# Performance work log

Hardware: AMD Instinct MI355X
Metric: run time of the kernel (lower is better)

Reference implementation:

```python
import jax, jax.numpy as jnp
import numpy as np
from jax.scipy.special import logsumexp

N = 4096          # nodes per graph
E = 65536         # edges per graph
HID = 128
HEADS = 4
HD = HID // HEADS
L_GNN = 2
L_CROSS = 3
SINK_ITERS = 20
LN_EPS = 1e-5
SCALE = 1.0 / np.sqrt(HD)


def layer_norm(x, g, b):
    m = jnp.mean(x, axis=-1, keepdims=True)
    v = jnp.mean((x - m) ** 2, axis=-1, keepdims=True)
    return (x - m) * jax.lax.rsqrt(v + LN_EPS) * g + b


def gcn_conv(x, ei, w, b):
    # PyG GCNConv: self-loops + symmetric normalization, sum aggregation
    n = x.shape[0]
    xl = x @ w                                  # [n, hid]
    loops = jnp.arange(n, dtype=ei.dtype)
    src = jnp.concatenate([ei[0], loops])
    dst = jnp.concatenate([ei[1], loops])
    deg = jax.ops.segment_sum(jnp.ones_like(src, dtype=x.dtype), dst, num_segments=n)
    dinv = jnp.where(deg > 0, jax.lax.rsqrt(deg), 0.0)
    norm = dinv[src] * dinv[dst]                # [E+n]
    msg = xl[src] * norm[:, None]
    return jax.ops.segment_sum(msg, dst, num_segments=n) + b


def encode(x, ei, gcn_w, gcn_b, ln_g, ln_b):
    h = x
    for l in range(L_GNN):
        h = gcn_conv(h, ei, gcn_w[l], gcn_b[l])
        h = layer_norm(h, ln_g[l], ln_b[l])
        h = jax.nn.relu(h)
    return h


def attend(X, Y, wq, wk, wv, wo, bo):
    # X attends to Y; residual add
    n, m = X.shape[0], Y.shape[0]
    Q = (X @ wq).reshape(n, HEADS, HD).transpose(1, 0, 2)   # [h, n, d]
    K = (Y @ wk).reshape(m, HEADS, HD).transpose(1, 0, 2)
    V = (Y @ wv).reshape(m, HEADS, HD).transpose(1, 0, 2)
    scores = jnp.einsum('hnd,hmd->hnm', Q, K) * SCALE
    attn = jax.nn.softmax(scores, axis=-1)
    O = jnp.einsum('hnm,hmd->hnd', attn, V)                 # [h, n, d]
    O = O.transpose(1, 0, 2).reshape(n, HID)
    return O @ wo + bo + X


def sinkhorn(log_alpha, n_iters=SINK_ITERS):
    def body(i, lp):
        lp = lp - logsumexp(lp, axis=1, keepdims=True)  # row normalize
        lp = lp - logsumexp(lp, axis=0, keepdims=True)  # col normalize
        return lp
    log_p = jax.lax.fori_loop(0, n_iters, body, log_alpha)
    return jnp.exp(log_p)


def setup_inputs() -> dict:
    key = jax.random.key(0)
    ks = jax.random.split(key, 24)
    f32 = jnp.float32
    w = lambda k, *s: jax.random.normal(k, s, dtype=f32) * 0.05
    inp = {
        'A_x': jax.random.normal(ks[0], (N, HID), dtype=f32),
        'A_ei': jax.random.randint(ks[1], (2, E), 0, N),
        'B_x': jax.random.normal(ks[2], (N, HID), dtype=f32),
        'B_ei': jax.random.randint(ks[3], (2, E), 0, N),
        'in_proj_w': w(ks[4], HID, HID),
        'in_proj_b': jnp.zeros((HID,), f32),
        'gcn_w': w(ks[5], L_GNN, HID, HID),
        'gcn_b': jnp.zeros((L_GNN, HID), f32),
        'gcn_ln_g': jnp.ones((L_GNN, HID), f32),
        'gcn_ln_b': jnp.zeros((L_GNN, HID), f32),
        'cross_q': w(ks[6], L_CROSS, HID, HID),
        'cross_k': w(ks[7], L_CROSS, HID, HID),
        'cross_v': w(ks[8], L_CROSS, HID, HID),
        'cross_o': w(ks[9], L_CROSS, HID, HID),
        'cross_o_b': jnp.zeros((L_CROSS, HID), f32),
        'post_ln_g': jnp.ones((HID,), f32),
        'post_ln_b': jnp.zeros((HID,), f32),
        'proj_w': w(ks[10], HID, HID),
        'proj_b': jnp.zeros((HID,), f32),
        'null_vec': jax.random.normal(ks[11], (HID,), dtype=f32) * 0.01,
        'cp_w1': w(ks[12], HID, HID),
        'cp_b1': jnp.zeros((HID,), f32),
        'cp_w2': w(ks[13], HID, HID),
        'cp_b2': jnp.zeros((HID,), f32),
    }
    return inp


def reference(A_x, A_ei, B_x, B_ei, in_proj_w, in_proj_b, gcn_w, gcn_b,
              gcn_ln_g, gcn_ln_b, cross_q, cross_k, cross_v, cross_o,
              cross_o_b, post_ln_g, post_ln_b, proj_w, proj_b, null_vec,
              cp_w1, cp_b1, cp_w2, cp_b2):
    A_in = A_x @ in_proj_w + in_proj_b
    B_in = B_x @ in_proj_w + in_proj_b
    A_h = encode(A_in, A_ei, gcn_w, gcn_b, gcn_ln_g, gcn_ln_b)
    B_h = encode(B_in, B_ei, gcn_w, gcn_b, gcn_ln_g, gcn_ln_b)
    for l in range(L_CROSS):
        A_new = attend(A_h, B_h, cross_q[l], cross_k[l], cross_v[l], cross_o[l], cross_o_b[l])
        B_new = attend(B_h, A_h, cross_q[l], cross_k[l], cross_v[l], cross_o[l], cross_o_b[l])
        A_h, B_h = A_new, B_new
    A_h = layer_norm(A_h, post_ln_g, post_ln_b)
    B_h = layer_norm(B_h, post_ln_g, post_ln_b)
    A_p = A_h @ proj_w + proj_b
    B_p = B_h @ proj_w + proj_b
    inv_sqrt_d = 1.0 / np.sqrt(HID)
    logits = (A_p @ B_p.T) * inv_sqrt_d                    # [N, N]
    null_col = (A_p @ null_vec) * inv_sqrt_d               # [N]
    logits_with_null = jnp.concatenate([logits, null_col[:, None]], axis=1)
    P = sinkhorn(logits_with_null)
    zA = jax.nn.relu(A_p @ cp_w1 + cp_b1) @ cp_w2 + cp_b2
    zB = jax.nn.relu(B_p @ cp_w1 + cp_b1) @ cp_w2 + cp_b2
    return (logits_with_null, P, zA, zB)
```

## Files before the change

### kernel.cpp

```cpp
#include <hip/hip_runtime.h>
#include <hip/hip_bf16.h>
#include <math.h>

#define NN 4096
#define EE 65536
#define HID_ 128
#define HDIM 32
#define NCOL 4097
#define EHP 4104

static constexpr float SCALE_ATT = 0.17677669529663687f;
static constexpr float INV_SQRT_D = 0.08838834764831845f;
static constexpr float LOG2E = 1.4426950408889634f;

typedef __attribute__((ext_vector_type(8))) short bf16x8;
typedef __attribute__((ext_vector_type(4))) float f32x4;
typedef _Float16 half8 __attribute__((ext_vector_type(8)));
typedef _Float16 half2v __attribute__((ext_vector_type(2)));

__device__ __forceinline__ float wred64(float v) {
#pragma unroll
  for (int m = 32; m > 0; m >>= 1) v += __shfl_xor(v, m, 64);
  return v;
}

__device__ __forceinline__ ushort f2b(float f) {
  __hip_bfloat16 h = __float2bfloat16(f);
  union { __hip_bfloat16 h; ushort u; } c;
  c.h = h;
  return c.u;
}

template <bool BIAS, bool RELU, bool RESID>
__global__ __launch_bounds__(256, 2) void gemm128_k(
    const float* __restrict__ x0, const float* __restrict__ x1,
    const float* __restrict__ w, const float* __restrict__ bias,
    const float* __restrict__ res0, const float* __restrict__ res1,
    float* __restrict__ o0, float* __restrict__ o1) {
  const float* x = blockIdx.y ? x1 : x0;
  const float* res = blockIdx.y ? res1 : res0;
  float* out = blockIdx.y ? o1 : o0;
  __shared__ float Xs[32][132];
  __shared__ float Ws[32][128];
  const int tid = threadIdx.x;
  const int rowbase = blockIdx.x * 32;
#pragma unroll
  for (int i = 0; i < 4; ++i) {
    int lin = tid + i * 256;
    int r = lin >> 5, c4 = lin & 31;
    *(float4*)&Xs[r][c4 * 4] =
        *(const float4*)&x[(size_t)(rowbase + r) * HID_ + c4 * 4];
  }
  float acc[4][4] = {};
  const int tr = tid >> 5, tc = tid & 31;
  const int r0 = tr * 4, c0 = tc * 4;
  for (int k0 = 0; k0 < 128; k0 += 32) {
    __syncthreads();
#pragma unroll
    for (int i = 0; i < 4; ++i) {
      int lin = tid + i * 256;
      int r = lin >> 5, c4 = lin & 31;
      *(float4*)&Ws[r][c4 * 4] =
          *(const float4*)&w[(size_t)(k0 + r) * HID_ + c4 * 4];
    }
    __syncthreads();
#pragma unroll
    for (int kk = 0; kk < 32; kk += 4) {
      float4 wv0 = *(const float4*)&Ws[kk + 0][c0];
      float4 wv1 = *(const float4*)&Ws[kk + 1][c0];
      float4 wv2 = *(const float4*)&Ws[kk + 2][c0];
      float4 wv3 = *(const float4*)&Ws[kk + 3][c0];
#pragma unroll
      for (int r = 0; r < 4; ++r) {
        float4 xv = *(const float4*)&Xs[r0 + r][k0 + kk];
        acc[r][0] += xv.x * wv0.x + xv.y * wv1.x + xv.z * wv2.x + xv.w * wv3.x;
        acc[r][1] += xv.x * wv0.y + xv.y * wv1.y + xv.z * wv2.y + xv.w * wv3.y;
        acc[r][2] += xv.x * wv0.z + xv.y * wv1.z + xv.z * wv2.z + xv.w * wv3.z;
        acc[r][3] += xv.x * wv0.w + xv.y * wv1.w + xv.z * wv2.w + xv.w * wv3.w;
      }
    }
  }
  float4 bv = make_float4(0.f, 0.f, 0.f, 0.f);
  if (BIAS) bv = *(const float4*)&bias[c0];
#pragma unroll
  for (int r = 0; r < 4; ++r) {
    size_t orow = (size_t)(rowbase + r0 + r) * HID_ + c0;
    float4 ov;
    ov.x = acc[r][0] + bv.x;
    ov.y = acc[r][1] + bv.y;
    ov.z = acc[r][2] + bv.z;
    ov.w = acc[r][3] + bv.w;
    if (RESID) {
      float4 rv = *(const float4*)&res[orow];
      ov.x += rv.x; ov.y += rv.y; ov.z += rv.z; ov.w += rv.w;
    }
    if (RELU) {
      ov.x = fmaxf(ov.x, 0.f); ov.y = fmaxf(ov.y, 0.f);
      ov.z = fmaxf(ov.z, 0.f); ov.w = fmaxf(ov.w, 0.f);
    }
    *(float4*)&out[orow] = ov;
  }
}

template <int MODE>
__global__ __launch_bounds__(256, 2) void gemm128_bf16_k(
    const float* __restrict__ x0, const float* __restrict__ x1,
    const float* __restrict__ w, float scale, ushort* __restrict__ o0,
    ushort* __restrict__ o1) {
  const float* x = blockIdx.y ? x1 : x0;
  ushort* out = blockIdx.y ? o1 : o0;
  __shared__ float Xs[32][132];
  __shared__ float Ws[32][128];
  const int tid = threadIdx.x;
  const int rowbase = blockIdx.x * 32;
#pragma unroll
  for (int i = 0; i < 4; ++i) {
    int lin = tid + i * 256;
    int r = lin >> 5, c4 = lin & 31;
    *(float4*)&Xs[r][c4 * 4] =
        *(const float4*)&x[(size_t)(rowbase + r) * HID_ + c4 * 4];
  }
  float acc[4][4] = {};
  const int tr = tid >> 5, tc = tid & 31;
  const int r0 = tr * 4, c0 = tc * 4;
  for (int k0 = 0; k0 < 128; k0 += 32) {
    __syncthreads();
#pragma unroll
    for (int i = 0; i < 4; ++i) {
      int lin = tid + i * 256;
      int r = lin >> 5, c4 = lin & 31;
      *(float4*)&Ws[r][c4 * 4] =
          *(const float4*)&w[(size_t)(k0 + r) * HID_ + c4 * 4];
    }
    __syncthreads();
#pragma unroll
    for (int kk = 0; kk < 32; kk += 4) {
      float4 wv0 = *(const float4*)&Ws[kk + 0][c0];
      float4 wv1 = *(const float4*)&Ws[kk + 1][c0];
      float4 wv2 = *(const float4*)&Ws[kk + 2][c0];
      float4 wv3 = *(const float4*)&Ws[kk + 3][c0];
#pragma unroll
      for (int r = 0; r < 4; ++r) {
        float4 xv = *(const float4*)&Xs[r0 + r][k0 + kk];
        acc[r][0] += xv.x * wv0.x + xv.y * wv1.x + xv.z * wv2.x + xv.w * wv3.x;
        acc[r][1] += xv.x * wv0.y + xv.y * wv1.y + xv.z * wv2.y + xv.w * wv3.y;
        acc[r][2] += xv.x * wv0.z + xv.y * wv1.z + xv.z * wv2.z + xv.w * wv3.z;
        acc[r][3] += xv.x * wv0.w + xv.y * wv1.w + xv.z * wv2.w + xv.w * wv3.w;
      }
    }
  }
  if (MODE == 0) {
#pragma unroll
    for (int r = 0; r < 4; ++r) {
      ushort4 pk = make_ushort4(
          f2b(acc[r][0] * scale), f2b(acc[r][1] * scale),
          f2b(acc[r][2] * scale), f2b(acc[r][3] * scale));
      *(ushort4*)&out[(size_t)(rowbase + r0 + r) * HID_ + c0] = pk;
    }
  } else {
#pragma unroll
    for (int r = 0; r < 4; ++r)
#pragma unroll
      for (int c = 0; c < 4; ++c)
        out[(size_t)(c0 + c) * NN + rowbase + r0 + r] = f2b(acc[r][c]);
  }
}

__global__ void count_deg_k(const int* __restrict__ eiA,
                            const int* __restrict__ eiB, int* cntA, int* cntB) {
  int e = blockIdx.x * 256 + threadIdx.x;
  const int* ei = blockIdx.y ? eiB : eiA;
  int* cnt = blockIdx.y ? cntB : cntA;
  atomicAdd(&cnt[ei[EE + e]], 1);
}

__global__ __launch_bounds__(1024) void scan_k(const int* cntA, const int* cntB,
                                               int* rpA, int* rpB, float* dinvA,
                                               float* dinvB) {
  const int* cnt = blockIdx.y ? cntB : cntA;
  int* rp = blockIdx.y ? rpB : rpA;
  float* dinv = blockIdx.y ? dinvB : dinvA;
  __shared__ int part[1024];
  int tid = threadIdx.x;
  int v0 = cnt[tid * 4], v1 = cnt[tid * 4 + 1], v2 = cnt[tid * 4 + 2],
      v3 = cnt[tid * 4 + 3];
  int tot = v0 + v1 + v2 + v3;
  part[tid] = tot;
  __syncthreads();
  int x = tot;
  for (int off = 1; off < 1024; off <<= 1) {
    int y = (tid >= off) ? part[tid - off] : 0;
    __syncthreads();
    x += y;
    part[tid] = x;
    __syncthreads();
  }
  int excl = x - tot;
  rp[tid * 4] = excl;
  rp[tid * 4 + 1] = excl + v0;
  rp[tid * 4 + 2] = excl + v0 + v1;
  rp[tid * 4 + 3] = excl + v0 + v1 + v2;
  if (tid == 1023) rp[4096] = x;
  dinv[tid * 4] = rsqrtf((float)(v0 + 1));
  dinv[tid * 4 + 1] = rsqrtf((float)(v1 + 1));
  dinv[tid * 4 + 2] = rsqrtf((float)(v2 + 1));
  dinv[tid * 4 + 3] = rsqrtf((float)(v3 + 1));
}

__global__ void fill_k(const int* __restrict__ eiA, const int* __restrict__ eiB,
                       const int* rpA, const int* rpB, int* fillA, int* fillB,
                       int* srcA, int* srcB) {
  int e = blockIdx.x * 256 + threadIdx.x;
  const int* ei = blockIdx.y ? eiB : eiA;
  const int* rp = blockIdx.y ? rpB : rpA;
  int* fill = blockIdx.y ? fillB : fillA;
  int* src = blockIdx.y ? srcB : srcA;
  int d = ei[EE + e], s = ei[e];
  int pos = atomicAdd(&fill[d], 1);
  src[rp[d] + pos] = s;
}

__global__ __launch_bounds__(256) void gcn_agg_k(
    const float* __restrict__ xlA, const float* __restrict__ xlB,
    const int* __restrict__ rpA, const int* __restrict__ rpB,
    const int* __restrict__ srcA, const int* __restrict__ srcB,
    const float* __restrict__ dinvA, const float* __restrict__ dinvB,
    const float* __restrict__ gb, const float* __restrict__ lg,
    const float* __restrict__ lb, float* __restrict__ outA,
    float* __restrict__ outB) {
  const float* xl = blockIdx.y ? xlB : xlA;
  const int* rp = blockIdx.y ? rpB : rpA;
  const int* src = blockIdx.y ? srcB : srcA;
  const float* dinv = blockIdx.y ? dinvB : dinvA;
  float* out = blockIdx.y ? outB : outA;
  int wid = threadIdx.x >> 6, lane = threadIdx.x & 63;
  int node = blockIdx.x * 4 + wid;
  int b = rp[node], e = rp[node + 1];
  float di = dinv[node];
  float a0 = 0.f, a1 = 0.f;
  for (int base = b; base < e; base += 64) {
    int rem = e - base;
    int sv = 0;
    float wv = 0.f;
    if (lane < rem) {
      int s = src[base + lane];
      sv = s;
      wv = dinv[s] * di;
    }
    int nch = rem < 64 ? rem : 64;
    for (int j = 0; j < nch; ++j) {
      int s = __shfl(sv, j, 64);
      float w = __shfl(wv, j, 64);
      a0 += xl[(size_t)s * HID_ + lane] * w;
      a1 += xl[(size_t)s * HID_ + 64 + lane] * w;
    }
  }
  a0 += xl[(size_t)node * HID_ + lane] * di * di;
  a1 += xl[(size_t)node * HID_ + 64 + lane] * di * di;
  a0 += gb[lane];
  a1 += gb[64 + lane];
  float mean = wred64(a0 + a1) * (1.f / 128.f);
  float d0 = a0 - mean, d1 = a1 - mean;
  float var = wred64(d0 * d0 + d1 * d1) * (1.f / 128.f);
  float rs = rsqrtf(var + 1e-5f);
  float o0 = d0 * rs * lg[lane] + lb[lane];
  float o1 = d1 * rs * lg[64 + lane] + lb[64 + lane];
  out[(size_t)node * HID_ + lane] = fmaxf(o0, 0.f);
  out[(size_t)node * HID_ + 64 + lane] = fmaxf(o1, 0.f);
}

__global__ __launch_bounds__(256) void ln_k(float* __restrict__ hA,
                                            float* __restrict__ hB,
                                            const float* __restrict__ g,
                                            const float* __restrict__ b) {
  float* h = blockIdx.y ? hB : hA;
  int wid = threadIdx.x >> 6, lane = threadIdx.x & 63;
  int row = blockIdx.x * 4 + wid;
  float a0 = h[(size_t)row * HID_ + lane];
  float a1 = h[(size_t)row * HID_ + 64 + lane];
  float mean = wred64(a0 + a1) * (1.f / 128.f);
  float d0 = a0 - mean, d1 = a1 - mean;
  float var = wred64(d0 * d0 + d1 * d1) * (1.f / 128.f);
  float rs = rsqrtf(var + 1e-5f);
  h[(size_t)row * HID_ + lane] = d0 * rs * g[lane] + b[lane];
  h[(size_t)row * HID_ + 64 + lane] = d1 * rs * g[64 + lane] + b[64 + lane];
}

__global__ __launch_bounds__(256, 2) void attn_mfma_k(
    const ushort* __restrict__ QA, const ushort* __restrict__ KA,
    const ushort* __restrict__ VtA, const ushort* __restrict__ QB,
    const ushort* __restrict__ KB, const ushort* __restrict__ VtB,
    float* __restrict__ outA, float* __restrict__ outB) {
  const int qt = blockIdx.x, h = blockIdx.y, dir = blockIdx.z;
  const ushort* Q = dir ? QB : QA;
  const ushort* K = dir ? KA : KB;
  const ushort* Vt = dir ? VtA : VtB;
  float* out = dir ? outB : outA;

  __shared__ ushort KF[2048];
  __shared__ ushort VF[2048];
  __shared__ ushort PF[4][1024];

  const int tid = threadIdx.x;
  const int w = tid >> 6, l = tid & 63;
  const int lr = l & 15, lg = l >> 4;

  const int qrow = qt * 64 + w * 16 + lr;
  bf16x8 qf = *(const bf16x8*)&Q[(size_t)qrow * HID_ + h * HDIM + lg * 8];

  f32x4 oacc0 = {0.f, 0.f, 0.f, 0.f};
  f32x4 oacc1 = {0.f, 0.f, 0.f, 0.f};
  float lpart = 0.f;

  const int ldst = ((w * 4 + lg) * 16 + lr) * 8;
  const ushort* Kg = K + (size_t)(w * 16 + lr) * HID_ + h * HDIM + lg * 8;
  const ushort* Vg =
      Vt + (size_t)(h * HDIM + (w >> 1) * 16 + lr) * NN + (w & 1) * 32 + lg * 8;

  for (int t = 0; t < 64; ++t) {
    const int kv0 = t * 64;
    __syncthreads();
    *(bf16x8*)&KF[ldst] = *(const bf16x8*)&Kg[(size_t)kv0 * HID_];
    *(bf16x8*)&VF[ldst] = *(const bf16x8*)&Vg[kv0];
    __syncthreads();
#pragma unroll
    for (int s = 0; s < 4; ++s) {
      bf16x8 kf = *(const bf16x8*)&KF[((s * 4 + lg) * 16 + lr) * 8];
      f32x4 c = {0.f, 0.f, 0.f, 0.f};
      c = __builtin_amdgcn_mfma_f32_16x16x32_bf16(kf, qf, c, 0, 0, 0);
      float e0 = exp2f(c[0]), e1 = exp2f(c[1]);
      float e2 = exp2f(c[2]), e3 = exp2f(c[3]);
      lpart += (e0 + e1) + (e2 + e3);
      ushort4 pk = make_ushort4(f2b(e0), f2b(e1), f2b(e2), f2b(e3));
      const int k0 = s >> 1;
      const int lgr = (s & 1) * 2 + (lg >> 1);
      const int e8 = (lg & 1) * 4;
      *(ushort4*)&PF[w][((k0 * 4 + lgr) * 16 + lr) * 8 + e8] = pk;
    }
#pragma unroll
    for (int k0 = 0; k0 < 2; ++k0) {
      bf16x8 pa = *(const bf16x8*)&PF[w][((k0 * 4 + lg) * 16 + lr) * 8];
      bf16x8 vb0 = *(const bf16x8*)&VF[((k0 * 4 + lg) * 16 + lr) * 8];
      bf16x8 vb1 = *(const bf16x8*)&VF[(((2 + k0) * 4 + lg) * 16 + lr) * 8];
      oacc0 = __builtin_amdgcn_mfma_f32_16x16x32_bf16(pa, vb0, oacc0, 0, 0, 0);
      oacc1 = __builtin_amdgcn_mfma_f32_16x16x32_bf16(pa, vb1, oacc1, 0, 0, 0);
    }
  }
  lpart += __shfl_xor(lpart, 16, 64);
  lpart += __shfl_xor(lpart, 32, 64);
#pragma unroll
  for (int r = 0; r < 4; ++r) {
    int q = qt * 64 + w * 16 + lg * 4 + r;
    float ls = __shfl(lpart, lg * 4 + r, 64);
    float inv = 1.f / ls;
    out[(size_t)q * HID_ + h * HDIM + lr] = oacc0[r] * inv;
    out[(size_t)q * HID_ + h * HDIM + 16 + lr] = oacc1[r] * inv;
  }
}

__global__ void castf2b_k(const float* __restrict__ A,
                          const float* __restrict__ B, ushort* __restrict__ Ab,
                          ushort* __restrict__ Bb) {
  int i = (blockIdx.x * 256 + threadIdx.x) * 8;
  float4 a0 = *(const float4*)&A[i];
  float4 a1 = *(const float4*)&A[i + 4];
  *(ushort4*)&Ab[i] = make_ushort4(f2b(a0.x), f2b(a0.y), f2b(a0.z), f2b(a0.w));
  *(ushort4*)&Ab[i + 4] =
      make_ushort4(f2b(a1.x), f2b(a1.y), f2b(a1.z), f2b(a1.w));
  float4 b0 = *(const float4*)&B[i];
  float4 b1 = *(const float4*)&B[i + 4];
  *(ushort4*)&Bb[i] = make_ushort4(f2b(b0.x), f2b(b0.y), f2b(b0.z), f2b(b0.w));
  *(ushort4*)&Bb[i + 4] =
      make_ushort4(f2b(b1.x), f2b(b1.y), f2b(b1.z), f2b(b1.w));
}

__global__ __launch_bounds__(256, 2) void gemm_nt_mfma_k(
    const ushort* __restrict__ Apb, const ushort* __restrict__ Bpb,
    float* __restrict__ L, _Float16* __restrict__ Eh) {
  __shared__ ushort As[128 * 128];
  __shared__ ushort Bs[128 * 128];
  const int tid = threadIdx.x;
  const int ab = blockIdx.y * 128, bb = blockIdx.x * 128;
#pragma unroll
  for (int i = 0; i < 8; ++i) {
    int lin = tid + i * 256;
    int row = lin >> 4, ch = lin & 15;
    int pch = ch ^ (row & 15);
    *(bf16x8*)&As[row * 128 + pch * 8] =
        *(const bf16x8*)&Apb[(size_t)(ab + row) * HID_ + ch * 8];
    *(bf16x8*)&Bs[row * 128 + pch * 8] =
        *(const bf16x8*)&Bpb[(size_t)(bb + row) * HID_ + ch * 8];
  }
  __syncthreads();
  const int w = tid >> 6, l = tid & 63, lr = l & 15, lg = l >> 4;
  f32x4 acc[2][8];
#pragma unroll
  for (int fm = 0; fm < 2; ++fm)
#pragma unroll
    for (int nf = 0; nf < 8; ++nf) acc[fm][nf] = {0.f, 0.f, 0.f, 0.f};
#pragma unroll
  for (int kc = 0; kc < 4; ++kc) {
    bf16x8 a0 = *(const bf16x8*)
        &As[((w * 2 + 0) * 16 + lr) * 128 + ((kc * 4 + lg) ^ lr) * 8];
    bf16x8 a1 = *(const bf16x8*)
        &As[((w * 2 + 1) * 16 + lr) * 128 + ((kc * 4 + lg) ^ lr) * 8];
#pragma unroll
    for (int nf = 0; nf < 8; ++nf) {
      bf16x8 bf = *(const bf16x8*)
          &Bs[(nf * 16 + lr) * 128 + ((kc * 4 + lg) ^ lr) * 8];
      acc[0][nf] = __builtin_amdgcn_mfma_f32_16x16x32_bf16(a0, bf, acc[0][nf], 0, 0, 0);
      acc[1][nf] = __builtin_amdgcn_mfma_f32_16x16x32_bf16(a1, bf, acc[1][nf], 0, 0, 0);
    }
  }
#pragma unroll
  for (int fm = 0; fm < 2; ++fm)
#pragma unroll
    for (int nf = 0; nf < 8; ++nf)
#pragma unroll
      for (int r = 0; r < 4; ++r) {
        int row = ab + (w * 2 + fm) * 16 + lg * 4 + r;
        int col = bb + nf * 16 + lr;
        float v = acc[fm][nf][r] * INV_SQRT_D;
        L[(size_t)row * NCOL + col] = v;
        Eh[(size_t)row * EHP + col] = (_Float16)exp2f(v * LOG2E);
      }
}

__global__ void null_col_k(const float* __restrict__ Ap,
                           const float* __restrict__ nv, float* __restrict__ L,
                           _Float16* __restrict__ Eh) {
  int row = blockIdx.x, lane = threadIdx.x;
  float s = Ap[(size_t)row * HID_ + lane] * nv[lane] +
            Ap[(size_t)row * HID_ + 64 + lane] * nv[64 + lane];
  s = wred64(s);
  if (lane == 0) {
    float v = s * INV_SQRT_D;
    L[(size_t)row * NCOL + 4096] = v;
    Eh[(size_t)row * EHP + 4096] = (_Float16)exp2f(v * LOG2E);
  }
  if (lane >= 1 && lane < 8) Eh[(size_t)row * EHP + 4096 + lane] = (_Float16)0.f;
}

__global__ void sink_init_k(float* t0) {
  int j = blockIdx.x * 256 + threadIdx.x;
  if (j < EHP) t0[j] = 1.f;
}

__global__ __launch_bounds__(256) void sink_rowm_k(
    const _Float16* __restrict__ Eh, const float* __restrict__ t_old,
    float* __restrict__ t_new, float* __restrict__ u) {
  __shared__ float vls[EHP];
  int tid = threadIdx.x;
  if (blockIdx.x < 17) {
    int j = blockIdx.x * 256 + tid;
    if (j < EHP) t_new[j] = 0.f;
  }
  for (int i = tid; i < EHP; i += 256)
    vls[i] = (i < NCOL) ? (1.f / t_old[i]) : 0.f;
  __syncthreads();
  int w = tid >> 6, l = tid & 63;
  for (int rr = 0; rr < 4; ++rr) {
    int row = blockIdx.x * 16 + w * 4 + rr;
    const _Float16* Ep = Eh + (size_t)row * EHP;
    float s = 0.f;
    for (int j = l * 8; j < EHP; j += 512) {
      half8 e = *(const half8*)&Ep[j];
#pragma unroll
      for (int k = 0; k < 8; ++k) s += (float)e[k] * vls[j + k];
    }
    s = wred64(s);
    if (l == 0) u[row] = 1.f / s;
  }
}

__global__ __launch_bounds__(256) void sink_colm_k(
    const _Float16* __restrict__ Eh, const float* __restrict__ u,
    float* __restrict__ t_new) {
  __shared__ float uls[64];
  int tid = threadIdx.x;
  int i0 = blockIdx.y * 64;
  if (tid < 64) uls[tid] = u[i0 + tid];
  __syncthreads();
  int j0 = (blockIdx.x * 256 + tid) * 2;
  if (j0 >= EHP) return;
  float s0 = 0.f, s1 = 0.f;
#pragma unroll 8
  for (int i = 0; i < 64; ++i) {
    half2v e = *(const half2v*)&Eh[(size_t)(i0 + i) * EHP + j0];
    s0 += (float)e[0] * uls[i];
    s1 += (float)e[1] * uls[i];
  }
  atomicAdd(&t_new[j0], s0);
  atomicAdd(&t_new[j0 + 1], s1);
}

__global__ __launch_bounds__(256) void sink_finalE_k(
    const _Float16* __restrict__ Eh, const float* __restrict__ u,
    const float* __restrict__ t, float* __restrict__ P) {
  __shared__ float vls[NCOL];
  int tid = threadIdx.x, row = blockIdx.x;
  for (int i = tid; i < NCOL; i += 256) vls[i] = 1.f / t[i];
  __syncthreads();
  float ur = u[row];
  const _Float16* Ep = Eh + (size_t)row * EHP;
  float* Pp = P + (size_t)row * NCOL;
  for (int j = tid; j < NCOL; j += 256) Pp[j] = (float)Ep[j] * ur * vls[j];
}

extern "C" void kernel_launch(void* const* d_in, const int* in_sizes, int n_in,
                              void* d_out, int out_size, void* d_ws,
                              size_t ws_size, hipStream_t stream) {
  const float* A_x = (const float*)d_in[0];
  const int* A_ei = (const int*)d_in[1];
  const float* B_x = (const float*)d_in[2];
  const int* B_ei = (const int*)d_in[3];
  const float* in_w = (const float*)d_in[4];
  const float* in_b = (const float*)d_in[5];
  const float* gcn_w = (const float*)d_in[6];
  const float* gcn_b = (const float*)d_in[7];
  const float* lng = (const float*)d_in[8];
  const float* lnb = (const float*)d_in[9];
  const float* cq = (const float*)d_in[10];
  const float* ck = (const float*)d_in[11];
  const float* cv = (const float*)d_in[12];
  const float* co = (const float*)d_in[13];
  const float* cob = (const float*)d_in[14];
  const float* plg = (const float*)d_in[15];
  const float* plb = (const float*)d_in[16];
  const float* pw = (const float*)d_in[17];
  const float* pb = (const float*)d_in[18];
  const float* nullv = (const float*)d_in[19];
  const float* w1 = (const float*)d_in[20];
  const float* b1 = (const float*)d_in[21];
  const float* w2 = (const float*)d_in[22];
  const float* b2 = (const float*)d_in[23];

  float* ws = (float*)d_ws;
  size_t off = 0;
  auto alloc = [&](size_t n) { float* p = ws + off; off += n; return p; };
  const size_t NHE = (size_t)NN * HID_;
  float* tA = alloc(NHE);
  float* tB = alloc(NHE);
  float* Ap = alloc(NHE);
  float* Bp = alloc(NHE);
  ushort* Apb = (ushort*)alloc(NHE / 2);
  ushort* Bpb = (ushort*)alloc(NHE / 2);
  float* uvec = alloc(NN);
  float* t0 = alloc(EHP);
  float* t1 = alloc(EHP);
  float* zone = ws + off;
  float* hA0 = alloc(NHE); float* hB0 = alloc(NHE);
  float* hA1 = alloc(NHE); float* hB1 = alloc(NHE);
  float* QA = alloc(NHE);  float* KAb = alloc(NHE); float* VAb = alloc(NHE);
  float* QB = alloc(NHE);  float* KBb = alloc(NHE); float* VBb = alloc(NHE);
  float* dinvA = alloc(NN); float* dinvB = alloc(NN);
  int* ib = (int*)(ws + off);
  int* cntA = ib;             int* cntB = cntA + NN;
  int* fillA = cntB + NN;     int* fillB = fillA + NN;
  int* rpA = fillB + NN;      int* rpB = rpA + (NN + 1);
  int* srcA = rpB + (NN + 1); int* srcB = srcA + EE;
  _Float16* Eh = (_Float16*)zone;
  {
    size_t zone_used = (size_t)(ws + off - zone) + (2 * EE + 4 * NN + 2 * (NN + 1)) / 1;
    size_t eh_floats = ((size_t)NN * EHP + 1) / 2;
    size_t zone_named = (size_t)((ws + off) - zone);
    (void)zone_used; (void)zone_named;
    size_t ints_floats = (size_t)(4 * NN + 2 * (NN + 1) + 2 * EE);
    size_t named = (size_t)((ws + off) - zone) + ints_floats;
    size_t need = eh_floats > named ? eh_floats : named;
    off = (size_t)(zone - ws) + need;
  }

  float* Lout = (float*)d_out;
  float* Pout = Lout + (size_t)NN * NCOL;
  float* zA = Pout + (size_t)NN * NCOL;
  float* zB = zA + NHE;

  hipMemsetAsync(cntA, 0, 4 * NN * sizeof(int), stream);

  gemm128_k<true, false, false><<<dim3(128, 2), 256, 0, stream>>>(
      A_x, B_x, in_w, in_b, nullptr, nullptr, hA0, hB0);
  count_deg_k<<<dim3(256, 2), 256, 0, stream>>>(A_ei, B_ei, cntA, cntB);
  scan_k<<<dim3(1, 2), 1024, 0, stream>>>(cntA, cntB, rpA, rpB, dinvA, dinvB);
  fill_k<<<dim3(256, 2), 256, 0, stream>>>(A_ei, B_ei, rpA, rpB, fillA, fillB,
                                           srcA, srcB);
  float* hA = hA0; float* hB = hB0; float* aA = hA1; float* aB = hB1;
  for (int l = 0; l < 2; ++l) {
    gemm128_k<false, false, false><<<dim3(128, 2), 256, 0, stream>>>(
        hA, hB, gcn_w + (size_t)l * HID_ * HID_, nullptr, nullptr, nullptr, tA,
        tB);
    gcn_agg_k<<<dim3(1024, 2), 256, 0, stream>>>(
        tA, tB, rpA, rpB, srcA, srcB, dinvA, dinvB, gcn_b + l * HID_,
        lng + l * HID_, lnb + l * HID_, hA, hB);
  }
  for (int l = 0; l < 3; ++l) {
    const float* wq = cq + (size_t)l * HID_ * HID_;
    const float* wk = ck + (size_t)l * HID_ * HID_;
    const float* wv = cv + (size_t)l * HID_ * HID_;
    const float* wo = co + (size_t)l * HID_ * HID_;
    gemm128_bf16_k<0><<<dim3(128, 2), 256, 0, stream>>>(
        hA, hB, wq, SCALE_ATT * LOG2E, (ushort*)QA, (ushort*)QB);
    gemm128_bf16_k<0><<<dim3(128, 2), 256, 0, stream>>>(
        hA, hB, wk, 1.f, (ushort*)KAb, (ushort*)KBb);
    gemm128_bf16_k<1><<<dim3(128, 2), 256, 0, stream>>>(
        hA, hB, wv, 1.f, (ushort*)VAb, (ushort*)VBb);
    attn_mfma_k<<<dim3(64, 4, 2), 256, 0, stream>>>(
        (ushort*)QA, (ushort*)KAb, (ushort*)VAb, (ushort*)QB, (ushort*)KBb,
        (ushort*)VBb, tA, tB);
    gemm128_k<true, false, true><<<dim3(128, 2), 256, 0, stream>>>(
        tA, tB, wo, cob + l * HID_, hA, hB, aA, aB);
    float* t;
    t = hA; hA = aA; aA = t;
    t = hB; hB = aB; aB = t;
  }
  ln_k<<<dim3(1024, 2), 256, 0, stream>>>(hA, hB, plg, plb);
  gemm128_k<true, false, false><<<dim3(128, 2), 256, 0, stream>>>(
      hA, hB, pw, pb, nullptr, nullptr, Ap, Bp);
  castf2b_k<<<256, 256, 0, stream>>>(Ap, Bp, Apb, Bpb);
  gemm_nt_mfma_k<<<dim3(32, 32), 256, 0, stream>>>(Apb, Bpb, Lout, Eh);
  null_col_k<<<NN, 64, 0, stream>>>(Ap, nullv, Lout, Eh);
  sink_init_k<<<17, 256, 0, stream>>>(t0);
  float* tcur = t0; float* tnext = t1;
  for (int it = 0; it < 20; ++it) {
    sink_rowm_k<<<256, 256, 0, stream>>>(Eh, tcur, tnext, uvec);
    sink_colm_k<<<dim3(9, 64), 256, 0, stream>>>(Eh, uvec, tnext);
    float* tt = tcur; tcur = tnext; tnext = tt;
  }
  sink_finalE_k<<<NN, 256, 0, stream>>>(Eh, uvec, tcur, Pout);
  gemm128_k<true, true, false><<<dim3(128, 2), 256, 0, stream>>>(
      Ap, Bp, w1, b1, nullptr, nullptr, tA, tB);
  gemm128_k<true, false, false><<<dim3(128, 2), 256, 0, stream>>>(
      tA, tB, w2, b2, nullptr, nullptr, zA, zB);
}
```

Measured before the change: 1.121 ms.

## Fuse QKV gemms, split-KV attention, fused Sinkhorn iteration, fold bf16 cast

Merges the three Q/K/V projection launches into one grid, splits the attention KV range in two with register prefetch and a separate combine kernel, and fuses the Sinkhorn row and column passes into a single kernel per iteration using a rotating triple buffer for the column sums. The bf16 cast of the projections is folded into the projection GEMM epilogue, and the P tile is packed with bit arithmetic. These cut launch count and extra passes over the 4096x4104 matrix, at the cost of partial-output traffic for split attention and more atomics in the column reduction.

```diff
diff --git a/kernel.cpp b/kernel.cpp
--- a/kernel.cpp
+++ b/kernel.cpp
@@ -16,7 +16,7 @@
 typedef __attribute__((ext_vector_type(8))) short bf16x8;
 typedef __attribute__((ext_vector_type(4))) float f32x4;
 typedef _Float16 half8 __attribute__((ext_vector_type(8)));
-typedef _Float16 half2v __attribute__((ext_vector_type(2)));
+typedef _Float16 half4v __attribute__((ext_vector_type(4)));
 
 __device__ __forceinline__ float wred64(float v) {
 #pragma unroll
@@ -31,15 +31,22 @@
   return c.u;
 }
 
-template <bool BIAS, bool RELU, bool RESID>
+__device__ __forceinline__ unsigned pack2bf(float e0, float e1) {
+  return ((__float_as_uint(e1) + 0x8000u) & 0xffff0000u) |
+         ((__float_as_uint(e0) + 0x8000u) >> 16);
+}
+
+template <bool BIAS, bool RELU, bool RESID, bool BCAST>
 __global__ __launch_bounds__(256, 2) void gemm128_k(
     const float* __restrict__ x0, const float* __restrict__ x1,
     const float* __restrict__ w, const float* __restrict__ bias,
     const float* __restrict__ res0, const float* __restrict__ res1,
-    float* __restrict__ o0, float* __restrict__ o1) {
+    float* __restrict__ o0, float* __restrict__ o1,
+    ushort* __restrict__ ob0, ushort* __restrict__ ob1) {
   const float* x = blockIdx.y ? x1 : x0;
   const float* res = blockIdx.y ? res1 : res0;
   float* out = blockIdx.y ? o1 : o0;
+  ushort* outb = blockIdx.y ? ob1 : ob0;
   __shared__ float Xs[32][132];
   __shared__ float Ws[32][128];
   const int tid = threadIdx.x;
@@ -99,16 +106,26 @@
       ov.z = fmaxf(ov.z, 0.f); ov.w = fmaxf(ov.w, 0.f);
     }
     *(float4*)&out[orow] = ov;
-  }
-}
-
-template <int MODE>
-__global__ __launch_bounds__(256, 2) void gemm128_bf16_k(
+    if (BCAST) {
+      *(ushort4*)&outb[orow] =
+          make_ushort4(f2b(ov.x), f2b(ov.y), f2b(ov.z), f2b(ov.w));
+    }
+  }
+}
+
+__global__ __launch_bounds__(256, 2) void gemm_qkv_k(
     const float* __restrict__ x0, const float* __restrict__ x1,
-    const float* __restrict__ w, float scale, ushort* __restrict__ o0,
-    ushort* __restrict__ o1) {
+    const float* __restrict__ wq, const float* __restrict__ wk,
+    const float* __restrict__ wv, ushort* __restrict__ QA,
+    ushort* __restrict__ QB, ushort* __restrict__ KA, ushort* __restrict__ KB,
+    ushort* __restrict__ VA, ushort* __restrict__ VB) {
+  const int z = blockIdx.z;
   const float* x = blockIdx.y ? x1 : x0;
-  ushort* out = blockIdx.y ? o1 : o0;
+  const float* w = (z == 0) ? wq : (z == 1 ? wk : wv);
+  ushort* out = (z == 0) ? (blockIdx.y ? QB : QA)
+                         : (z == 1 ? (blockIdx.y ? KB : KA)
+                                   : (blockIdx.y ? VB : VA));
+  const float scale = (z == 0) ? SCALE_ATT * LOG2E : 1.f;
   __shared__ float Xs[32][132];
   __shared__ float Ws[32][128];
   const int tid = threadIdx.x;
@@ -149,7 +166,7 @@
       }
     }
   }
-  if (MODE == 0) {
+  if (z < 2) {
 #pragma unroll
     for (int r = 0; r < 4; ++r) {
       ushort4 pk = make_ushort4(
@@ -286,16 +303,16 @@
   h[(size_t)row * HID_ + 64 + lane] = d1 * rs * g[64 + lane] + b[64 + lane];
 }
 
-__global__ __launch_bounds__(256, 2) void attn_mfma_k(
+__global__ __launch_bounds__(256, 4) void attn_mfma_k(
     const ushort* __restrict__ QA, const ushort* __restrict__ KA,
     const ushort* __restrict__ VtA, const ushort* __restrict__ QB,
     const ushort* __restrict__ KB, const ushort* __restrict__ VtB,
-    float* __restrict__ outA, float* __restrict__ outB) {
-  const int qt = blockIdx.x, h = blockIdx.y, dir = blockIdx.z;
+    float* __restrict__ Opart, float* __restrict__ lpart) {
+  const int qt = blockIdx.x, h = blockIdx.y;
+  const int dir = blockIdx.z >> 1, sl = blockIdx.z & 1;
   const ushort* Q = dir ? QB : QA;
   const ushort* K = dir ? KA : KB;
   const ushort* Vt = dir ? VtA : VtB;
-  float* out = dir ? outB : outA;
 
   __shared__ ushort KF[2048];
   __shared__ ushort VF[2048];
@@ -310,18 +327,25 @@
 
   f32x4 oacc0 = {0.f, 0.f, 0.f, 0.f};
   f32x4 oacc1 = {0.f, 0.f, 0.f, 0.f};
-  float lpart = 0.f;
+  float lsum = 0.f;
 
   const int ldst = ((w * 4 + lg) * 16 + lr) * 8;
-  const ushort* Kg = K + (size_t)(w * 16 + lr) * HID_ + h * HDIM + lg * 8;
-  const ushort* Vg =
-      Vt + (size_t)(h * HDIM + (w >> 1) * 16 + lr) * NN + (w & 1) * 32 + lg * 8;
-
-  for (int t = 0; t < 64; ++t) {
-    const int kv0 = t * 64;
-    __syncthreads();
-    *(bf16x8*)&KF[ldst] = *(const bf16x8*)&Kg[(size_t)kv0 * HID_];
-    *(bf16x8*)&VF[ldst] = *(const bf16x8*)&Vg[kv0];
+  const ushort* Kg =
+      K + (size_t)(sl * 2048 + w * 16 + lr) * HID_ + h * HDIM + lg * 8;
+  const ushort* Vg = Vt + (size_t)(h * HDIM + (w >> 1) * 16 + lr) * NN +
+                     sl * 2048 + (w & 1) * 32 + lg * 8;
+
+  bf16x8 kreg = *(const bf16x8*)Kg;
+  bf16x8 vreg = *(const bf16x8*)Vg;
+
+  for (int t = 0; t < 32; ++t) {
+    __syncthreads();
+    *(bf16x8*)&KF[ldst] = kreg;
+    *(bf16x8*)&VF[ldst] = vreg;
+    if (t < 31) {
+      kreg = *(const bf16x8*)&Kg[(size_t)(t + 1) * 64 * HID_];
+      vreg = *(const bf16x8*)&Vg[(t + 1) * 64];
+    }
     __syncthreads();
 #pragma unroll
     for (int s = 0; s < 4; ++s) {
@@ -330,12 +354,12 @@
       c = __builtin_amdgcn_mfma_f32_16x16x32_bf16(kf, qf, c, 0, 0, 0);
       float e0 = exp2f(c[0]), e1 = exp2f(c[1]);
       float e2 = exp2f(c[2]), e3 = exp2f(c[3]);
-      lpart += (e0 + e1) + (e2 + e3);
-      ushort4 pk = make_ushort4(f2b(e0), f2b(e1), f2b(e2), f2b(e3));
+      lsum += (e0 + e1) + (e2 + e3);
       const int k0 = s >> 1;
       const int lgr = (s & 1) * 2 + (lg >> 1);
       const int e8 = (lg & 1) * 4;
-      *(ushort4*)&PF[w][((k0 * 4 + lgr) * 16 + lr) * 8 + e8] = pk;
+      *(uint2*)&PF[w][((k0 * 4 + lgr) * 16 + lr) * 8 + e8] =
+          make_uint2(pack2bf(e0, e1), pack2bf(e2, e3));
     }
 #pragma unroll
     for (int k0 = 0; k0 < 2; ++k0) {
@@ -346,32 +370,34 @@
       oacc1 = __builtin_amdgcn_mfma_f32_16x16x32_bf16(pa, vb1, oacc1, 0, 0, 0);
     }
   }
-  lpart += __shfl_xor(lpart, 16, 64);
-  lpart += __shfl_xor(lpart, 32, 64);
+  lsum += __shfl_xor(lsum, 16, 64);
+  lsum += __shfl_xor(lsum, 32, 64);
+  const int pb = sl * 2 + dir;
+  if (lg == 0)
+    lpart[(size_t)(pb * 4 + h) * NN + qt * 64 + w * 16 + lr] = lsum;
 #pragma unroll
   for (int r = 0; r < 4; ++r) {
     int q = qt * 64 + w * 16 + lg * 4 + r;
-    float ls = __shfl(lpart, lg * 4 + r, 64);
-    float inv = 1.f / ls;
-    out[(size_t)q * HID_ + h * HDIM + lr] = oacc0[r] * inv;
-    out[(size_t)q * HID_ + h * HDIM + 16 + lr] = oacc1[r] * inv;
-  }
-}
-
-__global__ void castf2b_k(const float* __restrict__ A,
-                          const float* __restrict__ B, ushort* __restrict__ Ab,
-                          ushort* __restrict__ Bb) {
-  int i = (blockIdx.x * 256 + threadIdx.x) * 8;
-  float4 a0 = *(const float4*)&A[i];
-  float4 a1 = *(const float4*)&A[i + 4];
-  *(ushort4*)&Ab[i] = make_ushort4(f2b(a0.x), f2b(a0.y), f2b(a0.z), f2b(a0.w));
-  *(ushort4*)&Ab[i + 4] =
-      make_ushort4(f2b(a1.x), f2b(a1.y), f2b(a1.z), f2b(a1.w));
-  float4 b0 = *(const float4*)&B[i];
-  float4 b1 = *(const float4*)&B[i + 4];
-  *(ushort4*)&Bb[i] = make_ushort4(f2b(b0.x), f2b(b0.y), f2b(b0.z), f2b(b0.w));
-  *(ushort4*)&Bb[i + 4] =
-      make_ushort4(f2b(b1.x), f2b(b1.y), f2b(b1.z), f2b(b1.w));
+    Opart[((size_t)pb * NN + q) * HID_ + h * HDIM + lr] = oacc0[r];
+    Opart[((size_t)pb * NN + q) * HID_ + h * HDIM + 16 + lr] = oacc1[r];
+  }
+}
+
+__global__ void attn_combine_k(const float* __restrict__ Opart,
+                               const float* __restrict__ lpart,
+                               float* __restrict__ outA,
+                               float* __restrict__ outB) {
+  int row = blockIdx.x, dir = blockIdx.y, f = threadIdx.x;
+  int h = f >> 5;
+  float o = 0.f, lsum = 0.f;
+#pragma unroll
+  for (int sl = 0; sl < 2; ++sl) {
+    int pb = sl * 2 + dir;
+    o += Opart[((size_t)pb * NN + row) * HID_ + f];
+    lsum += lpart[(size_t)(pb * 4 + h) * NN + row];
+  }
+  float* out = dir ? outB : outA;
+  out[(size_t)row * HID_ + f] = o / lsum;
 }
 
 __global__ __launch_bounds__(256, 2) void gemm_nt_mfma_k(
@@ -441,57 +467,67 @@
   if (lane >= 1 && lane < 8) Eh[(size_t)row * EHP + 4096 + lane] = (_Float16)0.f;
 }
 
-__global__ void sink_init_k(float* t0) {
-  int j = blockIdx.x * 256 + threadIdx.x;
-  if (j < EHP) t0[j] = 1.f;
-}
-
-__global__ __launch_bounds__(256) void sink_rowm_k(
+__global__ __launch_bounds__(256) void sink_iter_k(
     const _Float16* __restrict__ Eh, const float* __restrict__ t_old,
-    float* __restrict__ t_new, float* __restrict__ u) {
-  __shared__ float vls[EHP];
-  int tid = threadIdx.x;
-  if (blockIdx.x < 17) {
-    int j = blockIdx.x * 256 + tid;
-    if (j < EHP) t_new[j] = 0.f;
+    float* __restrict__ t_new, float* __restrict__ t_zero,
+    float* __restrict__ u) {
+  __shared__ float vinv[EHP];
+  __shared__ float uls[8];
+  const int tid = threadIdx.x, bid = blockIdx.x;
+  if (tid < 9) {
+    int z = bid * 9 + tid;
+    if (z < EHP) t_zero[z] = 0.f;
   }
   for (int i = tid; i < EHP; i += 256)
-    vls[i] = (i < NCOL) ? (1.f / t_old[i]) : 0.f;
+    vinv[i] = (i < NCOL) ? (1.f / t_old[i]) : 0.f;
   __syncthreads();
-  int w = tid >> 6, l = tid & 63;
-  for (int rr = 0; rr < 4; ++rr) {
-    int row = blockIdx.x * 16 + w * 4 + rr;
+  const int w = tid >> 6, l = tid & 63;
+  const int row0 = bid * 8;
+#pragma unroll
+  for (int rr = 0; rr < 2; ++rr) {
+    int row = row0 + w * 2 + rr;
     const _Float16* Ep = Eh + (size_t)row * EHP;
     float s = 0.f;
-    for (int j = l * 8; j < EHP; j += 512) {
-      half8 e = *(const half8*)&Ep[j];
-#pragma unroll
-      for (int k = 0; k < 8; ++k) s += (float)e[k] * vls[j + k];
+    for (int j = l * 4; j < EHP; j += 256) {
+      half4v e = *(const half4v*)&Ep[j];
+      float4 vv = *(const float4*)&vinv[j];
+      s += (float)e[0] * vv.x + (float)e[1] * vv.y + (float)e[2] * vv.z +
+           (float)e[3] * vv.w;
     }
     s = wred64(s);
-    if (l == 0) u[row] = 1.f / s;
-  }
-}
-
-__global__ __launch_bounds__(256) void sink_colm_k(
-    const _Float16* __restrict__ Eh, const float* __restrict__ u,
-    float* __restrict__ t_new) {
-  __shared__ float uls[64];
-  int tid = threadIdx.x;
-  int i0 = blockIdx.y * 64;
-  if (tid < 64) uls[tid] = u[i0 + tid];
+    if (l == 0) {
+      float uv = 1.f / s;
+      uls[w * 2 + rr] = uv;
+      u[row] = uv;
+    }
+  }
   __syncthreads();
-  int j0 = (blockIdx.x * 256 + tid) * 2;
-  if (j0 >= EHP) return;
-  float s0 = 0.f, s1 = 0.f;
-#pragma unroll 8
-  for (int i = 0; i < 64; ++i) {
-    half2v e = *(const half2v*)&Eh[(size_t)(i0 + i) * EHP + j0];
-    s0 += (float)e[0] * uls[i];
-    s1 += (float)e[1] * uls[i];
-  }
-  atomicAdd(&t_new[j0], s0);
-  atomicAdd(&t_new[j0 + 1], s1);
+  float ur[8];
+#pragma unroll
+  for (int r = 0; r < 8; ++r) ur[r] = uls[r];
+  for (int j = tid * 4; j < EHP; j += 1024) {
+    float a0 = 0.f, a1 = 0.f, a2 = 0.f, a3 = 0.f;
+#pragma unroll
+    for (int r = 0; r < 8; ++r) {
+      half4v e = *(const half4v*)&Eh[(size_t)(row0 + r) * EHP + j];
+      a0 += (float)e[0] * ur[r];
+      a1 += (float)e[1] * ur[r];
+      a2 += (float)e[2] * ur[r];
+      a3 += (float)e[3] * ur[r];
+    }
+    atomicAdd(&t_new[j + 0], a0);
+    atomicAdd(&t_new[j + 1], a1);
+    atomicAdd(&t_new[j + 2], a2);
+    atomicAdd(&t_new[j + 3], a3);
+  }
+}
+
+__global__ void sink_init_k(float* t0, float* t1) {
+  int j = blockIdx.x * 256 + threadIdx.x;
+  if (j < EHP) {
+    t0[j] = 1.f;
+    t1[j] = 0.f;
+  }
 }
 
 __global__ __launch_bounds__(256) void sink_finalE_k(
@@ -548,25 +584,25 @@
   float* uvec = alloc(NN);
   float* t0 = alloc(EHP);
   float* t1 = alloc(EHP);
+  float* t2 = alloc(EHP);
   float* zone = ws + off;
   float* hA0 = alloc(NHE); float* hB0 = alloc(NHE);
   float* hA1 = alloc(NHE); float* hB1 = alloc(NHE);
   float* QA = alloc(NHE);  float* KAb = alloc(NHE); float* VAb = alloc(NHE);
   float* QB = alloc(NHE);  float* KBb = alloc(NHE); float* VBb = alloc(NHE);
+  float* Opart = alloc(4 * NHE);
+  float* lpart = alloc((size_t)16 * NN);
   float* dinvA = alloc(NN); float* dinvB = alloc(NN);
   int* ib = (int*)(ws + off);
   int* cntA = ib;             int* cntB = cntA + NN;
   int* fillA = cntB + NN;     int* fillB = fillA + NN;
   int* rpA = fillB + NN;      int* rpB = rpA + (NN + 1);
   int* srcA = rpB + (NN + 1); int* srcB = srcA + EE;
+  size_t ints_floats = (size_t)(4 * NN + 2 * (NN + 1) + 2 * EE);
   _Float16* Eh = (_Float16*)zone;
   {
-    size_t zone_used = (size_t)(ws + off - zone) + (2 * EE + 4 * NN + 2 * (NN + 1)) / 1;
+    size_t named = (size_t)((ws + off) - zone) + ints_floats;
     size_t eh_floats = ((size_t)NN * EHP + 1) / 2;
-    size_t zone_named = (size_t)((ws + off) - zone);
-    (void)zone_used; (void)zone_named;
-    size_t ints_floats = (size_t)(4 * NN + 2 * (NN + 1) + 2 * EE);
-    size_t named = (size_t)((ws + off) - zone) + ints_floats;
     size_t need = eh_floats > named ? eh_floats : named;
     off = (size_t)(zone - ws) + need;
   }
@@ -578,17 +614,17 @@
 
   hipMemsetAsync(cntA, 0, 4 * NN * sizeof(int), stream);
 
-  gemm128_k<true, false, false><<<dim3(128, 2), 256, 0, stream>>>(
-      A_x, B_x, in_w, in_b, nullptr, nullptr, hA0, hB0);
+  gemm128_k<true, false, false, false><<<dim3(128, 2), 256, 0, stream>>>(
+      A_x, B_x, in_w, in_b, nullptr, nullptr, hA0, hB0, nullptr, nullptr);
   count_deg_k<<<dim3(256, 2), 256, 0, stream>>>(A_ei, B_ei, cntA, cntB);
   scan_k<<<dim3(1, 2), 1024, 0, stream>>>(cntA, cntB, rpA, rpB, dinvA, dinvB);
   fill_k<<<dim3(256, 2), 256, 0, stream>>>(A_ei, B_ei, rpA, rpB, fillA, fillB,
                                            srcA, srcB);
   float* hA = hA0; float* hB = hB0; float* aA = hA1; float* aB = hB1;
   for (int l = 0; l < 2; ++l) {
-    gemm128_k<false, false, false><<<dim3(128, 2), 256, 0, stream>>>(
+    gemm128_k<false, false, false, false><<<dim3(128, 2), 256, 0, stream>>>(
         hA, hB, gcn_w + (size_t)l * HID_ * HID_, nullptr, nullptr, nullptr, tA,
-        tB);
+        tB, nullptr, nullptr);
     gcn_agg_k<<<dim3(1024, 2), 256, 0, stream>>>(
         tA, tB, rpA, rpB, srcA, srcB, dinvA, dinvB, gcn_b + l * HID_,
         lng + l * HID_, lnb + l * HID_, hA, hB);
@@ -598,37 +634,33 @@
     const float* wk = ck + (size_t)l * HID_ * HID_;
     const float* wv = cv + (size_t)l * HID_ * HID_;
     const float* wo = co + (size_t)l * HID_ * HID_;
-    gemm128_bf16_k<0><<<dim3(128, 2), 256, 0, stream>>>(
-        hA, hB, wq, SCALE_ATT * LOG2E, (ushort*)QA, (ushort*)QB);
-    gemm128_bf16_k<0><<<dim3(128, 2), 256, 0, stream>>>(
-        hA, hB, wk, 1.f, (ushort*)KAb, (ushort*)KBb);
-    gemm128_bf16_k<1><<<dim3(128, 2), 256, 0, stream>>>(
-        hA, hB, wv, 1.f, (ushort*)VAb, (ushort*)VBb);
-    attn_mfma_k<<<dim3(64, 4, 2), 256, 0, stream>>>(
+    gemm_qkv_k<<<dim3(128, 2, 3), 256, 0, stream>>>(
+        hA, hB, wq, wk, wv, (ushort*)QA, (ushort*)QB, (ushort*)KAb,
+        (ushort*)KBb, (ushort*)VAb, (ushort*)VBb);
+    attn_mfma_k<<<dim3(64, 4, 4), 256, 0, stream>>>(
         (ushort*)QA, (ushort*)KAb, (ushort*)VAb, (ushort*)QB, (ushort*)KBb,
-        (ushort*)VBb, tA, tB);
-    gemm128_k<true, false, true><<<dim3(128, 2), 256, 0, stream>>>(
-        tA, tB, wo, cob + l * HID_, hA, hB, aA, aB);
+        (ushort*)VBb, Opart, lpart);
+    attn_combine_k<<<dim3(NN, 2), 128, 0, stream>>>(Opart, lpart, tA, tB);
+    gemm128_k<true, false, true, false><<<dim3(128, 2), 256, 0, stream>>>(
+        tA, tB, wo, cob + l * HID_, hA, hB, aA, aB, nullptr, nullptr);
     float* t;
     t = hA; hA = aA; aA = t;
     t = hB; hB = aB; aB = t;
   }
   ln_k<<<dim3(1024, 2), 256, 0, stream>>>(hA, hB, plg, plb);
-  gemm128_k<true, false, false><<<dim3(128, 2), 256, 0, stream>>>(
-      hA, hB, pw, pb, nullptr, nullptr, Ap, Bp);
-  castf2b_k<<<256, 256, 0, stream>>>(Ap, Bp, Apb, Bpb);
+  gemm128_k<true, false, false, true><<<dim3(128, 2), 256, 0, stream>>>(
+      hA, hB, pw, pb, nullptr, nullptr, Ap, Bp, Apb, Bpb);
   gemm_nt_mfma_k<<<dim3(32, 32), 256, 0, stream>>>(Apb, Bpb, Lout, Eh);
   null_col_k<<<NN, 64, 0, stream>>>(Ap, nullv, Lout, Eh);
-  sink_init_k<<<17, 256, 0, stream>>>(t0);
-  float* tcur = t0; float* tnext = t1;
+  sink_init_k<<<17, 256, 0, stream>>>(t0, t1);
+  float* tb[3] = {t0, t1, t2};
   for (int it = 0; it < 20; ++it) {
-    sink_rowm_k<<<256, 256, 0, stream>>>(Eh, tcur, tnext, uvec);
-    sink_colm_k<<<dim3(9, 64), 256, 0, stream>>>(Eh, uvec, tnext);
-    float* tt = tcur; tcur = tnext; tnext = tt;
-  }
-  sink_finalE_k<<<NN, 256, 0, stream>>>(Eh, uvec, tcur, Pout);
-  gemm128_k<true, true, false><<<dim3(128, 2), 256, 0, stream>>>(
-      Ap, Bp, w1, b1, nullptr, nullptr, tA, tB);
-  gemm128_k<true, false, false><<<dim3(128, 2), 256, 0, stream>>>(
-      tA, tB, w2, b2, nullptr, nullptr, zA, zB);
-}
+    sink_iter_k<<<512, 256, 0, stream>>>(Eh, tb[it % 3], tb[(it + 1) % 3],
+                                         tb[(it + 2) % 3], uvec);
+  }
+  sink_finalE_k<<<NN, 256, 0, stream>>>(Eh, uvec, tb[2], Pout);
+  gemm128_k<true, true, false, false><<<dim3(128, 2), 256, 0, stream>>>(
+      Ap, Bp, w1, b1, nullptr, nullptr, tA, tB, nullptr, nullptr);
+  gemm128_k<true, false, false, false><<<dim3(128, 2), 256, 0, stream>>>(
+      tA, tB, w2, b2, nullptr, nullptr, zA, zB, nullptr, nullptr);
+}
```

New measurement: 2.772 ms. +147.2%, slower.
